# Optimization experiments

Hardware: AMD Instinct MI355X
Metric: run time of the kernel (lower is better)

Reference implementation:

```python
import jax, jax.numpy as jnp
import numpy as np

D = 256

def setup_inputs() -> dict:
    key = jax.random.key(0)
    ks = jax.random.split(key, 7)
    B, N = 4, 4096
    s = 1.0 / np.sqrt(D)
    return {
        "x": jax.random.normal(ks[0], (B, D, N), dtype=jnp.float32),
        "Wq": jax.random.normal(ks[1], (D, D), dtype=jnp.float32) * s,
        "bq": jax.random.normal(ks[2], (D,), dtype=jnp.float32) * s,
        "Wk": jax.random.normal(ks[3], (D, D), dtype=jnp.float32) * s,
        "bk": jax.random.normal(ks[4], (D,), dtype=jnp.float32) * s,
        "Wv": jax.random.normal(ks[5], (D, D), dtype=jnp.float32) * s,
        "bv": jax.random.normal(ks[6], (D,), dtype=jnp.float32) * s,
    }


def reference(x, Wq, bq, Wk, bk, Wv, bv):
    # x: (B, D, N) -> xt: (B, N, D)
    xt = jnp.swapaxes(x, 1, 2)
    q = xt @ Wq + bq  # (B, N, D)
    k = xt @ Wk + bk
    v = xt @ Wv + bv
    # full N x N attention, NO 1/sqrt(d) scaling (matches original)
    attn = jnp.einsum("bnd,bmd->bnm", q, k)
    attn = jax.nn.softmax(attn, axis=-1)
    out = jnp.einsum("bnm,bmd->bnd", attn, v)  # (B, N, D)
    return jnp.swapaxes(out, 1, 2)  # (B, D, N)
```

## Files before the change

kernel.cpp:

```cpp
#include <hip/hip_runtime.h>
#include <math.h>

#define Dd 256
#define Nn 4096
#define Bb 4
#define BQ 128
#define BK 128
#define SPLIT 2

typedef _Float16 f16;
typedef _Float16 half8 __attribute__((ext_vector_type(8)));
typedef _Float16 half4 __attribute__((ext_vector_type(4)));
typedef float f32x4 __attribute__((ext_vector_type(4)));

#define LOG2E 1.4426950408889634f

template <int CTRL>
__device__ __forceinline__ float dppf(float x) {
    int r = __builtin_amdgcn_update_dpp(0, __builtin_bit_cast(int, x),
                                        CTRL, 0xF, 0xF, false);
    return __builtin_bit_cast(float, r);
}
__device__ __forceinline__ float red16_max(float x) {
    x = fmaxf(x, dppf<0x128>(x));
    x = fmaxf(x, dppf<0x124>(x));
    x = fmaxf(x, dppf<0x122>(x));
    x = fmaxf(x, dppf<0x121>(x));
    return x;
}
__device__ __forceinline__ float red16_sum(float x) {
    x += dppf<0x128>(x); x += dppf<0x124>(x);
    x += dppf<0x122>(x); x += dppf<0x121>(x);
    return x;
}

__global__ __launch_bounds__(256) void wtrans(
    const float* __restrict__ Wq, const float* __restrict__ Wk,
    const float* __restrict__ Wv, f16* __restrict__ Wt)
{
    __shared__ float ld[64][65];
    const int which = blockIdx.y;
    const float* W = which == 0 ? Wq : (which == 1 ? Wk : Wv);
    const int tr = (blockIdx.x >> 2) * 64;
    const int tc = (blockIdx.x & 3) * 64;
    const int t = threadIdx.x;
    #pragma unroll
    for (int i = 0; i < 16; ++i) {
        int u = t + i * 256, r = u >> 6, c = u & 63;
        ld[r][c] = W[(size_t)(tr + r) * Dd + tc + c];
    }
    __syncthreads();
    f16* Wo = Wt + (size_t)which * Dd * Dd;
    #pragma unroll
    for (int i = 0; i < 16; ++i) {
        int u = t + i * 256, cp = u >> 6, rp = u & 63;
        Wo[(size_t)(tc + cp) * Dd + tr + rp] = (f16)ld[rp][cp];
    }
}

__global__ __launch_bounds__(256) void qkv_fused(
    const float* __restrict__ x, const f16* __restrict__ Wt,
    const float* __restrict__ bq, const float* __restrict__ bk,
    const float* __restrict__ bv,
    f16* __restrict__ Qh, f16* __restrict__ Kh, f16* __restrict__ Vth)
{
    __shared__ __align__(16) f16 xT[64][264];

    const int t = threadIdx.x;
    const int wave = t >> 6, lane = t & 63, quad = lane >> 4, l15 = lane & 15;
    const int n0  = blockIdx.x * 64;
    const int ch  = blockIdx.y;
    const int b   = blockIdx.z;
    const int col0 = ch * 128 + wave * 32;

    const float* xb = x + (size_t)b * Dd * Nn;
    #pragma unroll
    for (int i = 0; i < 16; ++i) {
        int u = t + i * 256, d = u >> 4, nq = (u & 15) * 4;
        float4 v4 = *(const float4*)&xb[(size_t)d * Nn + n0 + nq];
        xT[nq + 0][d] = (f16)v4.x; xT[nq + 1][d] = (f16)v4.y;
        xT[nq + 2][d] = (f16)v4.z; xT[nq + 3][d] = (f16)v4.w;
    }

    float bias[3][2];
    #pragma unroll
    for (int ct = 0; ct < 2; ++ct) {
        int col = col0 + ct * 16 + l15;
        bias[0][ct] = bq[col]; bias[1][ct] = bk[col]; bias[2][ct] = bv[col];
    }

    __syncthreads();

    #pragma unroll
    for (int which = 0; which < 3; ++which) {
        const f16* Wb = Wt + (size_t)which * Dd * Dd;
        half8 wf[2][8];
        #pragma unroll
        for (int ct = 0; ct < 2; ++ct)
            #pragma unroll
            for (int c = 0; c < 8; ++c)
                wf[ct][c] = *(const half8*)(Wb
                    + (size_t)(col0 + ct * 16 + l15) * Dd + c * 32 + quad * 8);

        f32x4 acc[4][2];
        #pragma unroll
        for (int rg = 0; rg < 4; ++rg) {
            acc[rg][0] = (f32x4){0.f, 0.f, 0.f, 0.f};
            acc[rg][1] = (f32x4){0.f, 0.f, 0.f, 0.f};
        }
        #pragma unroll
        for (int rg = 0; rg < 4; ++rg) {
            #pragma unroll
            for (int c = 0; c < 8; ++c) {
                half8 a = *(const half8*)&xT[rg * 16 + l15][c * 32 + quad * 8];
                acc[rg][0] = __builtin_amdgcn_mfma_f32_16x16x32_f16(
                    a, wf[0][c], acc[rg][0], 0, 0, 0);
                acc[rg][1] = __builtin_amdgcn_mfma_f32_16x16x32_f16(
                    a, wf[1][c], acc[rg][1], 0, 0, 0);
            }
        }

        if (which < 2) {
            f16* O = (which == 0 ? Qh : Kh) + ((size_t)b * Nn + n0) * Dd;
            #pragma unroll
            for (int rg = 0; rg < 4; ++rg) {
                #pragma unroll
                for (int ct = 0; ct < 2; ++ct) {
                    int col = col0 + ct * 16 + l15;
                    float bvv = bias[which][ct];
                    #pragma unroll
                    for (int r = 0; r < 4; ++r)
                        O[(size_t)(rg * 16 + quad * 4 + r) * Dd + col] =
                            (f16)(acc[rg][ct][r] + bvv);
                }
            }
        } else {
            f16* O = Vth + (size_t)b * Dd * Nn;
            #pragma unroll
            for (int rg = 0; rg < 4; ++rg) {
                #pragma unroll
                for (int ct = 0; ct < 2; ++ct) {
                    int col = col0 + ct * 16 + l15;
                    float bvv = bias[2][ct];
                    half4 o;
                    #pragma unroll
                    for (int r = 0; r < 4; ++r) o[r] = (f16)(acc[rg][ct][r] + bvv);
                    *(half4*)&O[(size_t)col * Nn + n0 + rg * 16 + quad * 4] = o;
                }
            }
        }
    }
}

__global__ __launch_bounds__(512, 2) void attn_mfma(
    const f16* __restrict__ Qh, const f16* __restrict__ Kh,
    const f16* __restrict__ Vth, f16* __restrict__ Opart,
    float* __restrict__ mpart, float* __restrict__ lpart)
{
    __shared__ __align__(16) f16 Ks[2][BK][264];
    __shared__ float alpha_s[8][16];
    __shared__ float l_sh[8][16];

    const int t    = threadIdx.x;
    const int wave = t >> 6, lane = t & 63;
    const int quad = lane >> 4, l15 = lane & 15;
    const int b    = blockIdx.y;
    const int s    = blockIdx.z;
    const int q0   = blockIdx.x * BQ;
    const int qw   = q0 + wave * 16;
    const int kvlen = Nn / SPLIT;
    const int kv0  = s * kvlen;

    half8 qf[8];
    const f16* Qrow = Qh + ((size_t)b * Nn + qw + l15) * Dd + quad * 8;
    #pragma unroll
    for (int c = 0; c < 8; ++c) {
        qf[c] = *(const half8*)(Qrow + c * 32);
        qf[c] = qf[c] * (f16)LOG2E;
    }

    f32x4 acc[16];
    #pragma unroll
    for (int n = 0; n < 16; ++n) acc[n] = (f32x4){0.f, 0.f, 0.f, 0.f};
    f32x4 m4 = {-1e30f, -1e30f, -1e30f, -1e30f};
    f32x4 l4 = {0.f, 0.f, 0.f, 0.f};

    const f16* Kb   = Kh + (size_t)b * Nn * Dd;
    const f16* Vrow = Vth + (size_t)b * Dd * Nn
                    + (size_t)(wave * 32 + l15) * Nn + quad * 8;

    #pragma unroll
    for (int i = 0; i < 8; ++i) {
        int u = t + i * 512;
        int r = u >> 5, c = u & 31;
        *(half8*)&Ks[0][r][c * 8] =
            *(const half8*)(Kb + (size_t)(kv0 + r) * Dd + c * 8);
    }
    __syncthreads();

    int buf = 0;
    for (int k0 = kv0; k0 < kv0 + kvlen; k0 += BK) {
        const int kn = k0 + BK;
        const bool havenext = kn < kv0 + kvlen;
        half8 kreg[8];
        if (havenext) {
            #pragma unroll
            for (int i = 0; i < 8; ++i) {
                int u = t + i * 512;
                int r = u >> 5, c = u & 31;
                kreg[i] = *(const half8*)(Kb + (size_t)(kn + r) * Dd + c * 8);
            }
        }

        half8 vbf[2][4];
        #pragma unroll
        for (int dt = 0; dt < 2; ++dt) {
            #pragma unroll
            for (int cbb = 0; cbb < 4; ++cbb)
                vbf[dt][cbb] = *(const half8*)(Vrow + (size_t)dt * 16 * Nn + k0 + cbb * 32);
        }

        f32x4 S[8];
        #pragma unroll
        for (int cb = 0; cb < 8; ++cb) S[cb] = (f32x4){0.f, 0.f, 0.f, 0.f};
        #pragma unroll
        for (int c = 0; c < 8; ++c) {
            #pragma unroll
            for (int cb = 0; cb < 8; ++cb) {
                half8 kb = *(const half8*)&Ks[buf][cb * 16 + l15][c * 32 + quad * 8];
                S[cb] = __builtin_amdgcn_mfma_f32_16x16x32_f16(qf[c], kb, S[cb], 0, 0, 0);
            }
        }

        f32x4 tmax = S[0];
        #pragma unroll
        for (int cb = 1; cb < 8; ++cb) {
            tmax.x = fmaxf(tmax.x, S[cb].x); tmax.y = fmaxf(tmax.y, S[cb].y);
            tmax.z = fmaxf(tmax.z, S[cb].z); tmax.w = fmaxf(tmax.w, S[cb].w);
        }
        tmax.x = red16_max(tmax.x); tmax.y = red16_max(tmax.y);
        tmax.z = red16_max(tmax.z); tmax.w = red16_max(tmax.w);
        f32x4 newm;
        newm.x = fmaxf(m4.x, tmax.x); newm.y = fmaxf(m4.y, tmax.y);
        newm.z = fmaxf(m4.z, tmax.z); newm.w = fmaxf(m4.w, tmax.w);
        f32x4 al;
        al.x = __builtin_amdgcn_exp2f(m4.x - newm.x);
        al.y = __builtin_amdgcn_exp2f(m4.y - newm.y);
        al.z = __builtin_amdgcn_exp2f(m4.z - newm.z);
        al.w = __builtin_amdgcn_exp2f(m4.w - newm.w);
        #pragma unroll
        for (int cb = 0; cb < 8; ++cb) {
            S[cb].x = __builtin_amdgcn_exp2f(S[cb].x - newm.x);
            S[cb].y = __builtin_amdgcn_exp2f(S[cb].y - newm.y);
            S[cb].z = __builtin_amdgcn_exp2f(S[cb].z - newm.z);
            S[cb].w = __builtin_amdgcn_exp2f(S[cb].w - newm.w);
        }
        f32x4 rsum = S[0];
        #pragma unroll
        for (int cb = 1; cb < 8; ++cb) rsum += S[cb];
        rsum.x = red16_sum(rsum.x); rsum.y = red16_sum(rsum.y);
        rsum.z = red16_sum(rsum.z); rsum.w = red16_sum(rsum.w);
        l4 = l4 * al + rsum;
        m4 = newm;

        __syncthreads();

        f16 (*Ps)[16][136] = (f16 (*)[16][136])&Ks[buf][0][0];
        const int pr = quad * 4;
        #pragma unroll
        for (int cb = 0; cb < 8; ++cb) {
            Ps[wave][pr + 0][cb * 16 + l15] = (f16)S[cb].x;
            Ps[wave][pr + 1][cb * 16 + l15] = (f16)S[cb].y;
            Ps[wave][pr + 2][cb * 16 + l15] = (f16)S[cb].z;
            Ps[wave][pr + 3][cb * 16 + l15] = (f16)S[cb].w;
        }
        if (l15 == 0) {
            float4 a4 = {al.x, al.y, al.z, al.w};
            *(float4*)&alpha_s[wave][pr] = a4;
        }
        __syncthreads();

        float4 alq[8];
        int need = 0;
        #pragma unroll
        for (int qb = 0; qb < 8; ++qb) {
            alq[qb] = *(const float4*)&alpha_s[qb][pr];
            need |= (alq[qb].x != 1.f) | (alq[qb].y != 1.f) |
                    (alq[qb].z != 1.f) | (alq[qb].w != 1.f);
        }
        if (__any(need)) {
            #pragma unroll
            for (int qb = 0; qb < 8; ++qb) {
                f32x4 a = {alq[qb].x, alq[qb].y, alq[qb].z, alq[qb].w};
                acc[qb * 2 + 0] *= a;
                acc[qb * 2 + 1] *= a;
            }
        }

        #pragma unroll
        for (int qb = 0; qb < 8; ++qb) {
            #pragma unroll
            for (int cbb = 0; cbb < 4; ++cbb) {
                half8 ap = *(const half8*)&Ps[qb][l15][cbb * 32 + quad * 8];
                acc[qb * 2 + 0] = __builtin_amdgcn_mfma_f32_16x16x32_f16(
                    ap, vbf[0][cbb], acc[qb * 2 + 0], 0, 0, 0);
                acc[qb * 2 + 1] = __builtin_amdgcn_mfma_f32_16x16x32_f16(
                    ap, vbf[1][cbb], acc[qb * 2 + 1], 0, 0, 0);
            }
        }

        if (havenext) {
            #pragma unroll
            for (int i = 0; i < 8; ++i) {
                int u = t + i * 512;
                int r = u >> 5, c = u & 31;
                *(half8*)&Ks[buf ^ 1][r][c * 8] = kreg[i];
            }
            buf ^= 1;
        }
        __syncthreads();
    }

    if (l15 == 0) {
        const int pr = quad * 4;
        float4 lv = {l4.x, l4.y, l4.z, l4.w};
        *(float4*)&l_sh[wave][pr] = lv;
        float mv[4] = {m4.x, m4.y, m4.z, m4.w};
        float lvv[4] = {l4.x, l4.y, l4.z, l4.w};
        #pragma unroll
        for (int r = 0; r < 4; ++r) {
            int n = qw + pr + r;
            mpart[(size_t)(s * Bb + b) * Nn + n] = mv[r];
            lpart[(size_t)(s * Bb + b) * Nn + n] = lvv[r];
        }
    }
    __syncthreads();

    f16* Ob = Opart + (size_t)(s * Bb + b) * Dd * Nn;
    #pragma unroll
    for (int qb = 0; qb < 8; ++qb) {
        float4 lq = *(const float4*)&l_sh[qb][quad * 4];
        f32x4 inv = {1.f / lq.x, 1.f / lq.y, 1.f / lq.z, 1.f / lq.w};
        #pragma unroll
        for (int dt = 0; dt < 2; ++dt) {
            int d = wave * 32 + dt * 16 + l15;
            f32x4 o = acc[qb * 2 + dt] * inv;
            half4 oh;
            oh[0] = (f16)o.x; oh[1] = (f16)o.y; oh[2] = (f16)o.z; oh[3] = (f16)o.w;
            *(half4*)&Ob[(size_t)d * Nn + q0 + qb * 16 + quad * 4] = oh;
        }
    }
}

__global__ __launch_bounds__(256) void combine(
    const f16* __restrict__ Opart, const float* __restrict__ mpart,
    const float* __restrict__ lpart, float* __restrict__ out)
{
    const int t = threadIdx.x;
    const int n0 = (blockIdx.x * 256 + t) * 8;
    const int d = blockIdx.y, b = blockIdx.z;

    float m[SPLIT][8], l[SPLIT][8];
    #pragma unroll
    for (int s = 0; s < SPLIT; ++s) {
        size_t base = (size_t)(s * Bb + b) * Nn + n0;
        float4 a0 = *(const float4*)&mpart[base];
        float4 a1 = *(const float4*)&mpart[base + 4];
        float4 c0 = *(const float4*)&lpart[base];
        float4 c1 = *(const float4*)&lpart[base + 4];
        m[s][0]=a0.x; m[s][1]=a0.y; m[s][2]=a0.z; m[s][3]=a0.w;
        m[s][4]=a1.x; m[s][5]=a1.y; m[s][6]=a1.z; m[s][7]=a1.w;
        l[s][0]=c0.x; l[s][1]=c0.y; l[s][2]=c0.z; l[s][3]=c0.w;
        l[s][4]=c1.x; l[s][5]=c1.y; l[s][6]=c1.z; l[s][7]=c1.w;
    }
    float w[SPLIT][8];
    #pragma unroll
    for (int jx = 0; jx < 8; ++jx) {
        float M = m[0][jx];
        #pragma unroll
        for (int s = 1; s < SPLIT; ++s) M = fmaxf(M, m[s][jx]);
        float L = 0.f;
        #pragma unroll
        for (int s = 0; s < SPLIT; ++s) {
            float ws = l[s][jx] * __builtin_amdgcn_exp2f(m[s][jx] - M);
            w[s][jx] = ws; L += ws;
        }
        float invL = 1.f / L;
        #pragma unroll
        for (int s = 0; s < SPLIT; ++s) w[s][jx] *= invL;
    }

    float o[8];
    #pragma unroll
    for (int jx = 0; jx < 8; ++jx) o[jx] = 0.f;
    #pragma unroll
    for (int s = 0; s < SPLIT; ++s) {
        half8 h = *(const half8*)&Opart[((size_t)(s * Bb + b) * Dd + d) * Nn + n0];
        #pragma unroll
        for (int jx = 0; jx < 8; ++jx) o[jx] += w[s][jx] * (float)h[jx];
    }
    float* op = out + ((size_t)b * Dd + d) * Nn + n0;
    f32x4 o0 = {o[0], o[1], o[2], o[3]};
    f32x4 o1 = {o[4], o[5], o[6], o[7]};
    *(f32x4*)op = o0;
    *(f32x4*)(op + 4) = o1;
}

extern "C" void kernel_launch(void* const* d_in, const int* in_sizes, int n_in,
                              void* d_out, int out_size, void* d_ws, size_t ws_size,
                              hipStream_t stream) {
    const float* x  = (const float*)d_in[0];
    const float* Wq = (const float*)d_in[1];
    const float* bq = (const float*)d_in[2];
    const float* Wk = (const float*)d_in[3];
    const float* bk = (const float*)d_in[4];
    const float* Wv = (const float*)d_in[5];
    const float* bv = (const float*)d_in[6];
    float* out = (float*)d_out;

    f16* Qh    = (f16*)d_ws;
    f16* Kh    = Qh + (size_t)Bb * Nn * Dd;
    f16* Vth   = Kh + (size_t)Bb * Nn * Dd;
    f16* Wt    = Vth + (size_t)Bb * Nn * Dd;
    f16* Opart = Wt + (size_t)3 * Dd * Dd;
    float* mpart = (float*)(Opart + (size_t)SPLIT * Bb * Dd * Nn);
    float* lpart = mpart + (size_t)SPLIT * Bb * Nn;

    wtrans<<<dim3(16, 3), 256, 0, stream>>>(Wq, Wk, Wv, Wt);
    qkv_fused<<<dim3(Nn / 64, 2, Bb), 256, 0, stream>>>(
        x, Wt, bq, bk, bv, Qh, Kh, Vth);
    attn_mfma<<<dim3(Nn / BQ, Bb, SPLIT), 512, 0, stream>>>(
        Qh, Kh, Vth, Opart, mpart, lpart);
    combine<<<dim3(Nn / 2048, Dd, Bb), 256, 0, stream>>>(
        Opart, mpart, lpart, out);
}
```

Measured before the change: 209.4 us.

## Software-pipeline attention loop so PV of previous tile overlaps QK of next

Restructures the KV loop into a two-stage software pipeline. Each step now computes QK^T for the current tile and then runs the P·V MFMAs for the previous tile, whose P sits in the other LDS buffer. The step also writes the next K tile into that buffer after P is consumed, and a final epilogue handles the last P·V. This removes one barrier per tile and lets softmax work overlap the MFMAs. In exchange it holds two sets of V registers, which raises register pressure, and it relies on LDS buffer aliasing between K and P.

```diff
diff --git a/kernel.cpp b/kernel.cpp
--- a/kernel.cpp
+++ b/kernel.cpp
@@ -152,6 +152,134 @@
     }
 }
 
+template <bool FIRST>
+__device__ __forceinline__ void tile_step(
+    int k0, bool havenext,
+    const f16* __restrict__ Kb, const f16* __restrict__ Vrow,
+    const half8 (&qf)[8],
+    half8 (&vW)[2][4], half8 (&vR)[2][4],
+    f32x4 (&acc)[16], f32x4& m4, f32x4& l4,
+    f16 (*KsCur)[264], f16 (*KsOth)[264],
+    float (*alpha_sp)[16],
+    int t, int wave, int quad, int l15)
+{
+    const int kn = k0 + BK;
+    const int pr = quad * 4;
+
+    half8 kreg[8];
+    if (havenext) {
+        #pragma unroll
+        for (int i = 0; i < 8; ++i) {
+            int u = t + i * 512;
+            int r = u >> 5, c = u & 31;
+            kreg[i] = *(const half8*)(Kb + (size_t)(kn + r) * Dd + c * 8);
+        }
+    }
+    #pragma unroll
+    for (int dt = 0; dt < 2; ++dt)
+        #pragma unroll
+        for (int cbb = 0; cbb < 4; ++cbb)
+            vW[dt][cbb] = *(const half8*)(Vrow + (size_t)dt * 16 * Nn + k0 + cbb * 32);
+
+    f32x4 S[8];
+    #pragma unroll
+    for (int cb = 0; cb < 8; ++cb) S[cb] = (f32x4){0.f, 0.f, 0.f, 0.f};
+    #pragma unroll
+    for (int c = 0; c < 8; ++c) {
+        #pragma unroll
+        for (int cb = 0; cb < 8; ++cb) {
+            half8 kb = *(const half8*)&KsCur[cb * 16 + l15][c * 32 + quad * 8];
+            S[cb] = __builtin_amdgcn_mfma_f32_16x16x32_f16(qf[c], kb, S[cb], 0, 0, 0);
+        }
+    }
+
+    if (!FIRST) {
+        f16 (*Pp)[16][136] = (f16 (*)[16][136])&KsOth[0][0];
+        float4 alq[8];
+        int need = 0;
+        #pragma unroll
+        for (int qb = 0; qb < 8; ++qb) {
+            alq[qb] = *(const float4*)&alpha_sp[qb][pr];
+            need |= (alq[qb].x != 1.f) | (alq[qb].y != 1.f) |
+                    (alq[qb].z != 1.f) | (alq[qb].w != 1.f);
+        }
+        if (__any(need)) {
+            #pragma unroll
+            for (int qb = 0; qb < 8; ++qb) {
+                f32x4 a = {alq[qb].x, alq[qb].y, alq[qb].z, alq[qb].w};
+                acc[qb * 2 + 0] *= a;
+                acc[qb * 2 + 1] *= a;
+            }
+        }
+        #pragma unroll
+        for (int qb = 0; qb < 8; ++qb) {
+            #pragma unroll
+            for (int cbb = 0; cbb < 4; ++cbb) {
+                half8 ap = *(const half8*)&Pp[qb][l15][cbb * 32 + quad * 8];
+                acc[qb * 2 + 0] = __builtin_amdgcn_mfma_f32_16x16x32_f16(
+                    ap, vR[0][cbb], acc[qb * 2 + 0], 0, 0, 0);
+                acc[qb * 2 + 1] = __builtin_amdgcn_mfma_f32_16x16x32_f16(
+                    ap, vR[1][cbb], acc[qb * 2 + 1], 0, 0, 0);
+            }
+        }
+    }
+
+    f32x4 tmax = S[0];
+    #pragma unroll
+    for (int cb = 1; cb < 8; ++cb) {
+        tmax.x = fmaxf(tmax.x, S[cb].x); tmax.y = fmaxf(tmax.y, S[cb].y);
+        tmax.z = fmaxf(tmax.z, S[cb].z); tmax.w = fmaxf(tmax.w, S[cb].w);
+    }
+    tmax.x = red16_max(tmax.x); tmax.y = red16_max(tmax.y);
+    tmax.z = red16_max(tmax.z); tmax.w = red16_max(tmax.w);
+    f32x4 newm;
+    newm.x = fmaxf(m4.x, tmax.x); newm.y = fmaxf(m4.y, tmax.y);
+    newm.z = fmaxf(m4.z, tmax.z); newm.w = fmaxf(m4.w, tmax.w);
+    f32x4 al;
+    al.x = __builtin_amdgcn_exp2f(m4.x - newm.x);
+    al.y = __builtin_amdgcn_exp2f(m4.y - newm.y);
+    al.z = __builtin_amdgcn_exp2f(m4.z - newm.z);
+    al.w = __builtin_amdgcn_exp2f(m4.w - newm.w);
+    #pragma unroll
+    for (int cb = 0; cb < 8; ++cb) {
+        S[cb].x = __builtin_amdgcn_exp2f(S[cb].x - newm.x);
+        S[cb].y = __builtin_amdgcn_exp2f(S[cb].y - newm.y);
+        S[cb].z = __builtin_amdgcn_exp2f(S[cb].z - newm.z);
+        S[cb].w = __builtin_amdgcn_exp2f(S[cb].w - newm.w);
+    }
+    f32x4 rsum = S[0];
+    #pragma unroll
+    for (int cb = 1; cb < 8; ++cb) rsum += S[cb];
+    rsum.x = red16_sum(rsum.x); rsum.y = red16_sum(rsum.y);
+    rsum.z = red16_sum(rsum.z); rsum.w = red16_sum(rsum.w);
+    l4 = l4 * al + rsum;
+    m4 = newm;
+
+    __syncthreads();
+
+    f16 (*Ps)[16][136] = (f16 (*)[16][136])&KsCur[0][0];
+    #pragma unroll
+    for (int cb = 0; cb < 8; ++cb) {
+        Ps[wave][pr + 0][cb * 16 + l15] = (f16)S[cb].x;
+        Ps[wave][pr + 1][cb * 16 + l15] = (f16)S[cb].y;
+        Ps[wave][pr + 2][cb * 16 + l15] = (f16)S[cb].z;
+        Ps[wave][pr + 3][cb * 16 + l15] = (f16)S[cb].w;
+    }
+    if (l15 == 0) {
+        float4 a4 = {al.x, al.y, al.z, al.w};
+        *(float4*)&alpha_sp[wave][pr] = a4;
+    }
+    if (havenext) {
+        #pragma unroll
+        for (int i = 0; i < 8; ++i) {
+            int u = t + i * 512;
+            int r = u >> 5, c = u & 31;
+            *(half8*)&KsOth[r][c * 8] = kreg[i];
+        }
+    }
+    __syncthreads();
+}
+
 __global__ __launch_bounds__(512, 2) void attn_mfma(
     const f16* __restrict__ Qh, const f16* __restrict__ Kh,
     const f16* __restrict__ Vth, f16* __restrict__ Opart,
@@ -198,88 +326,25 @@
     }
     __syncthreads();
 
-    int buf = 0;
-    for (int k0 = kv0; k0 < kv0 + kvlen; k0 += BK) {
-        const int kn = k0 + BK;
-        const bool havenext = kn < kv0 + kvlen;
-        half8 kreg[8];
-        if (havenext) {
-            #pragma unroll
-            for (int i = 0; i < 8; ++i) {
-                int u = t + i * 512;
-                int r = u >> 5, c = u & 31;
-                kreg[i] = *(const half8*)(Kb + (size_t)(kn + r) * Dd + c * 8);
-            }
-        }
-
-        half8 vbf[2][4];
-        #pragma unroll
-        for (int dt = 0; dt < 2; ++dt) {
-            #pragma unroll
-            for (int cbb = 0; cbb < 4; ++cbb)
-                vbf[dt][cbb] = *(const half8*)(Vrow + (size_t)dt * 16 * Nn + k0 + cbb * 32);
-        }
-
-        f32x4 S[8];
-        #pragma unroll
-        for (int cb = 0; cb < 8; ++cb) S[cb] = (f32x4){0.f, 0.f, 0.f, 0.f};
-        #pragma unroll
-        for (int c = 0; c < 8; ++c) {
-            #pragma unroll
-            for (int cb = 0; cb < 8; ++cb) {
-                half8 kb = *(const half8*)&Ks[buf][cb * 16 + l15][c * 32 + quad * 8];
-                S[cb] = __builtin_amdgcn_mfma_f32_16x16x32_f16(qf[c], kb, S[cb], 0, 0, 0);
-            }
-        }
-
-        f32x4 tmax = S[0];
-        #pragma unroll
-        for (int cb = 1; cb < 8; ++cb) {
-            tmax.x = fmaxf(tmax.x, S[cb].x); tmax.y = fmaxf(tmax.y, S[cb].y);
-            tmax.z = fmaxf(tmax.z, S[cb].z); tmax.w = fmaxf(tmax.w, S[cb].w);
-        }
-        tmax.x = red16_max(tmax.x); tmax.y = red16_max(tmax.y);
-        tmax.z = red16_max(tmax.z); tmax.w = red16_max(tmax.w);
-        f32x4 newm;
-        newm.x = fmaxf(m4.x, tmax.x); newm.y = fmaxf(m4.y, tmax.y);
-        newm.z = fmaxf(m4.z, tmax.z); newm.w = fmaxf(m4.w, tmax.w);
-        f32x4 al;
-        al.x = __builtin_amdgcn_exp2f(m4.x - newm.x);
-        al.y = __builtin_amdgcn_exp2f(m4.y - newm.y);
-        al.z = __builtin_amdgcn_exp2f(m4.z - newm.z);
-        al.w = __builtin_amdgcn_exp2f(m4.w - newm.w);
-        #pragma unroll
-        for (int cb = 0; cb < 8; ++cb) {
-            S[cb].x = __builtin_amdgcn_exp2f(S[cb].x - newm.x);
-            S[cb].y = __builtin_amdgcn_exp2f(S[cb].y - newm.y);
-            S[cb].z = __builtin_amdgcn_exp2f(S[cb].z - newm.z);
-            S[cb].w = __builtin_amdgcn_exp2f(S[cb].w - newm.w);
-        }
-        f32x4 rsum = S[0];
-        #pragma unroll
-        for (int cb = 1; cb < 8; ++cb) rsum += S[cb];
-        rsum.x = red16_sum(rsum.x); rsum.y = red16_sum(rsum.y);
-        rsum.z = red16_sum(rsum.z); rsum.w = red16_sum(rsum.w);
-        l4 = l4 * al + rsum;
-        m4 = newm;
-
-        __syncthreads();
-
-        f16 (*Ps)[16][136] = (f16 (*)[16][136])&Ks[buf][0][0];
+    half8 vA[2][4], vB[2][4];
+    f16 (*Ks0)[264] = Ks[0];
+    f16 (*Ks1)[264] = Ks[1];
+
+    for (int p = 0; p < 16; p += 2) {
+        int k0 = kv0 + p * BK;
+        if (p == 0)
+            tile_step<true >(k0, true, Kb, Vrow, qf, vA, vB, acc, m4, l4,
+                             Ks0, Ks1, alpha_s, t, wave, quad, l15);
+        else
+            tile_step<false>(k0, true, Kb, Vrow, qf, vA, vB, acc, m4, l4,
+                             Ks0, Ks1, alpha_s, t, wave, quad, l15);
+        tile_step<false>(k0 + BK, p + 2 < 16, Kb, Vrow, qf, vB, vA, acc, m4, l4,
+                         Ks1, Ks0, alpha_s, t, wave, quad, l15);
+    }
+
+    {
         const int pr = quad * 4;
-        #pragma unroll
-        for (int cb = 0; cb < 8; ++cb) {
-            Ps[wave][pr + 0][cb * 16 + l15] = (f16)S[cb].x;
-            Ps[wave][pr + 1][cb * 16 + l15] = (f16)S[cb].y;
-            Ps[wave][pr + 2][cb * 16 + l15] = (f16)S[cb].z;
-            Ps[wave][pr + 3][cb * 16 + l15] = (f16)S[cb].w;
-        }
-        if (l15 == 0) {
-            float4 a4 = {al.x, al.y, al.z, al.w};
-            *(float4*)&alpha_s[wave][pr] = a4;
-        }
-        __syncthreads();
-
+        f16 (*Pp)[16][136] = (f16 (*)[16][136])&Ks1[0][0];
         float4 alq[8];
         int need = 0;
         #pragma unroll
@@ -296,29 +361,17 @@
                 acc[qb * 2 + 1] *= a;
             }
         }
-
         #pragma unroll
         for (int qb = 0; qb < 8; ++qb) {
             #pragma unroll
             for (int cbb = 0; cbb < 4; ++cbb) {
-                half8 ap = *(const half8*)&Ps[qb][l15][cbb * 32 + quad * 8];
+                half8 ap = *(const half8*)&Pp[qb][l15][cbb * 32 + quad * 8];
                 acc[qb * 2 + 0] = __builtin_amdgcn_mfma_f32_16x16x32_f16(
-                    ap, vbf[0][cbb], acc[qb * 2 + 0], 0, 0, 0);
+                    ap, vB[0][cbb], acc[qb * 2 + 0], 0, 0, 0);
                 acc[qb * 2 + 1] = __builtin_amdgcn_mfma_f32_16x16x32_f16(
-                    ap, vbf[1][cbb], acc[qb * 2 + 1], 0, 0, 0);
-            }
-        }
-
-        if (havenext) {
-            #pragma unroll
-            for (int i = 0; i < 8; ++i) {
-                int u = t + i * 512;
-                int r = u >> 5, c = u & 31;
-                *(half8*)&Ks[buf ^ 1][r][c * 8] = kreg[i];
-            }
-            buf ^= 1;
-        }
-        __syncthreads();
+                    ap, vB[1][cbb], acc[qb * 2 + 1], 0, 0, 0);
+            }
+        }
     }
 
     if (l15 == 0) {
```

After: 430.8 us. +105.7%, slower.
